# Kernel optimization log

Measured on AMD Instinct MI355X. Metric: run time of the kernel, lower is better.

## Reference

```python
import jax, jax.numpy as jnp
import numpy as np

T, B, E, H = 2048, 2, 1024, 16
HD = E // H

def setup_inputs() -> dict:
    key = jax.random.key(0)
    k1, k2, k3 = jax.random.split(key, 3)
    x = jax.random.normal(k1, (T, B, E), dtype=jnp.float32)
    # xavier-uniform-like scale for weights
    in_proj_w = jax.random.normal(k2, (3 * E, E), dtype=jnp.float32) * (2.0 / (4 * E)) ** 0.5
    in_proj_b = jnp.zeros((3 * E,), dtype=jnp.float32)
    out_w = jax.random.normal(k3, (E, E), dtype=jnp.float32) * (1.0 / E) ** 0.5
    out_b = jnp.zeros((E,), dtype=jnp.float32)
    return {"x": x, "in_proj_w": in_proj_w, "in_proj_b": in_proj_b, "out_w": out_w, "out_b": out_b}

def reference(x, in_proj_w, in_proj_b, out_w, out_b):
    t, b, e = x.shape
    scale = HD ** (-0.5)
    # fused QKV projection: F.linear(x, W, b) = x @ W.T + b
    qkv = x @ in_proj_w.T + in_proj_b            # [T, B, 3E]
    q, k, v = jnp.split(qkv, 3, axis=-1)         # each [T, B, E]
    q = q * scale
    # reshape to heads: [T, B, E] -> [B, H, T, HD]
    def to_heads(a):
        return a.reshape(t, b, H, HD).transpose(1, 2, 0, 3)
    qh, kh, vh = to_heads(q), to_heads(k), to_heads(v)
    # scores [B, H, T, T] -- full NxN materialization, same as torch.bmm
    scores = jnp.einsum('bhtd,bhsd->bhts', qh, kh)
    w = jax.nn.softmax(scores.astype(jnp.float32), axis=-1).astype(scores.dtype)
    attn = jnp.einsum('bhts,bhsd->bhtd', w, vh)  # [B, H, T, HD]
    attn = attn.transpose(2, 0, 1, 3).reshape(t, b, e)  # [T, B, E]
    attn = attn @ out_w.T + out_b
    attn_weights = w.sum(axis=1) / H             # [B, T, T] head-averaged
    return attn, attn_weights
```

## Files before the change

### kernel.cpp

```cpp
#include <hip/hip_runtime.h>
#include <hip/hip_bf16.h>
#include <cstdint>

#define T_DIM 2048
#define B_DIM 2
#define E_DIM 1024
#define H_DIM 16
#define HD_DIM 64
#define M_DIM 4096
#define N1_DIM 3072
#define QK_SCALE 0.125f

typedef __attribute__((ext_vector_type(8))) short bfrag;
typedef __attribute__((ext_vector_type(4))) float f32x4;

__device__ __forceinline__ short f2bf(float f) {
  union { float f; uint32_t u; } v; v.f = f;
  uint32_t r = v.u + 0x7fffu + ((v.u >> 16) & 1u);
  return (short)(r >> 16);
}
__device__ __forceinline__ float bf2f(short b) {
  union { uint32_t u; float f; } v; v.u = ((uint32_t)(uint16_t)b) << 16;
  return v.f;
}
__device__ __forceinline__ f32x4 mfma16(bfrag a, bfrag b, f32x4 c) {
  return __builtin_amdgcn_mfma_f32_16x16x32_bf16(a, b, c, 0, 0, 0);
}

__global__ void split_kernel(const float* __restrict__ in,
                             short* __restrict__ hi, short* __restrict__ lo, int n) {
  int i = blockIdx.x * blockDim.x + threadIdx.x;
  int stride = gridDim.x * blockDim.x;
  for (; i < n; i += stride) {
    float v = in[i];
    short h = f2bf(v);
    hi[i] = h;
    lo[i] = f2bf(v - bf2f(h));
  }
}

template<int N_T, int K_T, bool OUT_BF16, bool DO_SCALE>
__global__ __launch_bounds__(256) void gemm_split(
    const short* __restrict__ Ahi, const short* __restrict__ Alo,
    const short* __restrict__ Bhi, const short* __restrict__ Blo,
    const float* __restrict__ bias, void* __restrict__ Cout)
{
  constexpr int BK = 32;
  constexpr int LDT = BK + 8;
  __shared__ short As[2][128][LDT];
  __shared__ short Bs[2][128][LDT];

  const int m0 = blockIdx.y * 128;
  const int n0 = blockIdx.x * 128;
  const int tid = threadIdx.x;
  const int lane = tid & 63;
  const int wave = tid >> 6;
  const int wr = (wave >> 1) * 64;
  const int wc = (wave & 1) * 64;

  f32x4 acc[4][4];
#pragma unroll
  for (int i = 0; i < 4; ++i)
#pragma unroll
    for (int j = 0; j < 4; ++j) acc[i][j] = f32x4{0.f, 0.f, 0.f, 0.f};

  const int ldr = tid >> 1;
  const int ldc0 = (tid & 1) << 4;

  for (int k0 = 0; k0 < K_T; k0 += BK) {
    const size_t aoff = (size_t)(m0 + ldr) * K_T + k0 + ldc0;
    const size_t boff = (size_t)(n0 + ldr) * K_T + k0 + ldc0;
    bfrag ah0 = *(const bfrag*)(Ahi + aoff);
    bfrag ah1 = *(const bfrag*)(Ahi + aoff + 8);
    bfrag al0 = *(const bfrag*)(Alo + aoff);
    bfrag al1 = *(const bfrag*)(Alo + aoff + 8);
    bfrag bh0 = *(const bfrag*)(Bhi + boff);
    bfrag bh1 = *(const bfrag*)(Bhi + boff + 8);
    bfrag bl0 = *(const bfrag*)(Blo + boff);
    bfrag bl1 = *(const bfrag*)(Blo + boff + 8);
    __syncthreads();
    *(bfrag*)&As[0][ldr][ldc0]     = ah0;
    *(bfrag*)&As[0][ldr][ldc0 + 8] = ah1;
    *(bfrag*)&As[1][ldr][ldc0]     = al0;
    *(bfrag*)&As[1][ldr][ldc0 + 8] = al1;
    *(bfrag*)&Bs[0][ldr][ldc0]     = bh0;
    *(bfrag*)&Bs[0][ldr][ldc0 + 8] = bh1;
    *(bfrag*)&Bs[1][ldr][ldc0]     = bl0;
    *(bfrag*)&Bs[1][ldr][ldc0 + 8] = bl1;
    __syncthreads();

    const int fr = lane & 15;
    const int fk = (lane >> 4) << 3;
    bfrag afh[4], afl[4];
#pragma unroll
    for (int fi = 0; fi < 4; ++fi) {
      afh[fi] = *(const bfrag*)&As[0][wr + fi * 16 + fr][fk];
      afl[fi] = *(const bfrag*)&As[1][wr + fi * 16 + fr][fk];
    }
#pragma unroll
    for (int fj = 0; fj < 4; ++fj) {
      bfrag bfh = *(const bfrag*)&Bs[0][wc + fj * 16 + fr][fk];
      bfrag bfl = *(const bfrag*)&Bs[1][wc + fj * 16 + fr][fk];
#pragma unroll
      for (int fi = 0; fi < 4; ++fi) {
        acc[fi][fj] = mfma16(afh[fi], bfh, acc[fi][fj]);
        acc[fi][fj] = mfma16(afh[fi], bfl, acc[fi][fj]);
        acc[fi][fj] = mfma16(afl[fi], bfh, acc[fi][fj]);
      }
    }
  }

  const int cr = (lane >> 4) << 2;
  const int cc = lane & 15;
#pragma unroll
  for (int fi = 0; fi < 4; ++fi)
#pragma unroll
    for (int fj = 0; fj < 4; ++fj)
#pragma unroll
      for (int r = 0; r < 4; ++r) {
        int m = m0 + wr + fi * 16 + cr + r;
        int n = n0 + wc + fj * 16 + cc;
        float v = acc[fi][fj][r] + bias[n];
        if (DO_SCALE) { if (n < E_DIM) v *= QK_SCALE; }
        if (OUT_BF16) ((short*)Cout)[(size_t)m * N_T + n] = f2bf(v);
        else          ((float*)Cout)[(size_t)m * N_T + n] = v;
      }
}

__global__ __launch_bounds__(256) void attn_kernel(
    const short* __restrict__ qkv,
    float* __restrict__ linv_ws,
    short* __restrict__ ctx_hi, short* __restrict__ ctx_lo)
{
  __shared__ short Ks[64][72];
  __shared__ short Vt[64][72];
  __shared__ short Ps[64][72];
  __shared__ float l_lds[64];

  const int bh = blockIdx.x;
  const int b  = bh >> 4;
  const int h  = bh & 15;
  const int t0 = blockIdx.y * 64;
  const int tid  = threadIdx.x;
  const int lane = tid & 63;
  const int wave = tid >> 6;
  const int fr = lane & 15;
  const int fk = (lane >> 4) << 3;
  const int cr = (lane >> 4) << 2;

  const size_t qb = ((size_t)(t0 + wave * 16 + fr) * B_DIM + b) * N1_DIM + h * HD_DIM;
  const bfrag aq0 = *(const bfrag*)(qkv + qb + fk);
  const bfrag aq1 = *(const bfrag*)(qkv + qb + fk + 32);

  if (tid < 64) l_lds[tid] = 0.0f;

  f32x4 pv[4];
#pragma unroll
  for (int i = 0; i < 4; ++i) pv[i] = f32x4{0.f, 0.f, 0.f, 0.f};

  const int r  = tid >> 2;
  const int ds = (tid & 3) << 4;
  const int vc0 = (((r >> 3) ^ (ds >> 3)) << 3) | (r & 7);
  const int vc1 = (((r >> 3) ^ ((ds >> 3) + 1)) << 3) | (r & 7);

  const size_t kstep = ((size_t)64 * B_DIM) * N1_DIM;
  size_t kb = ((size_t)r * B_DIM + b) * N1_DIM + E_DIM + h * HD_DIM + ds;
  bfrag kv0 = *(const bfrag*)(qkv + kb);
  bfrag kv1 = *(const bfrag*)(qkv + kb + 8);
  bfrag vv0 = *(const bfrag*)(qkv + kb + E_DIM);
  bfrag vv1 = *(const bfrag*)(qkv + kb + E_DIM + 8);

  for (int st = 0; st < T_DIM / 64; ++st) {
    __syncthreads();
    *(bfrag*)&Ks[r][ds]     = kv0;
    *(bfrag*)&Ks[r][ds + 8] = kv1;
#pragma unroll
    for (int j = 0; j < 8; ++j) Vt[ds + j][vc0]     = vv0[j];
#pragma unroll
    for (int j = 0; j < 8; ++j) Vt[ds + 8 + j][vc1] = vv1[j];
    __syncthreads();

    f32x4 sacc[4];
    __builtin_amdgcn_s_setprio(1);
#pragma unroll
    for (int fs = 0; fs < 4; ++fs) {
      bfrag bk0 = *(const bfrag*)&Ks[fs * 16 + fr][fk];
      bfrag bk1 = *(const bfrag*)&Ks[fs * 16 + fr][fk + 32];
      f32x4 a = f32x4{0.f, 0.f, 0.f, 0.f};
      a = mfma16(aq0, bk0, a);
      a = mfma16(aq1, bk1, a);
      sacc[fs] = a;
    }
    __builtin_amdgcn_s_setprio(0);

    if (st + 1 < T_DIM / 64) {
      kb += kstep;
      kv0 = *(const bfrag*)(qkv + kb);
      kv1 = *(const bfrag*)(qkv + kb + 8);
      vv0 = *(const bfrag*)(qkv + kb + E_DIM);
      vv1 = *(const bfrag*)(qkv + kb + E_DIM + 8);
    }

    float rsum[4] = {0.f, 0.f, 0.f, 0.f};
#pragma unroll
    for (int fs = 0; fs < 4; ++fs) {
#pragma unroll
      for (int rr = 0; rr < 4; ++rr) {
        float p = __expf(sacc[fs][rr]);
        Ps[wave * 16 + cr + rr][fs * 16 + fr] = f2bf(p);
        rsum[rr] += p;
      }
    }
#pragma unroll
    for (int rr = 0; rr < 4; ++rr) {
      float v = rsum[rr];
      v += __shfl_xor(v, 1);
      v += __shfl_xor(v, 2);
      v += __shfl_xor(v, 4);
      v += __shfl_xor(v, 8);
      if (fr == 0) l_lds[wave * 16 + cr + rr] += v;
    }

    bfrag pa0 = *(const bfrag*)&Ps[wave * 16 + fr][fk];
    bfrag pa1 = *(const bfrag*)&Ps[wave * 16 + fr][fk + 32];
    __builtin_amdgcn_s_setprio(1);
#pragma unroll
    for (int fd = 0; fd < 4; ++fd) {
      const int R = fd * 16 + fr;
      const int sg = (R >> 3) & 7;
      bfrag bv0 = *(const bfrag*)&Vt[R][(((fk >> 3) ^ sg) << 3)];
      bfrag bv1 = *(const bfrag*)&Vt[R][((((fk >> 3) + 4) ^ sg) << 3)];
      pv[fd] = mfma16(pa0, bv0, pv[fd]);
      pv[fd] = mfma16(pa1, bv1, pv[fd]);
    }
    __builtin_amdgcn_s_setprio(0);
  }
  __syncthreads();

  if (tid < 64) linv_ws[(size_t)bh * T_DIM + t0 + tid] = 1.0f / l_lds[tid];
#pragma unroll
  for (int rr = 0; rr < 4; ++rr) {
    const int row = wave * 16 + cr + rr;
    const float inv = 1.0f / l_lds[row];
#pragma unroll
    for (int fd = 0; fd < 4; ++fd) {
      float v = pv[fd][rr] * inv;
      int d = fd * 16 + fr;
      size_t off = ((size_t)(t0 + row) * B_DIM + b) * E_DIM + h * HD_DIM + d;
      short hi = f2bf(v);
      ctx_hi[off] = hi;
      ctx_lo[off] = f2bf(v - bf2f(hi));
    }
  }
}

__global__ __launch_bounds__(256) void weights_kernel(
    const short* __restrict__ qkv, const float* __restrict__ linv,
    float* __restrict__ outw)
{
  __shared__ short Qs[64][72];
  __shared__ short Ks[64][72];
  __shared__ float Ls[16][64];

  const int s0 = blockIdx.x * 64;
  const int bt = blockIdx.y;
  const int b  = bt >> 5;
  const int t0 = (bt & 31) * 64;
  const int tid  = threadIdx.x;
  const int lane = tid & 63;
  const int wave = tid >> 6;
  const int fr = lane & 15;
  const int fk = (lane >> 4) << 3;
  const int cr = (lane >> 4) << 2;

  {
    const int h  = tid >> 4;
    const int r4 = (tid & 15) << 2;
    float4 v = *(const float4*)(linv + (size_t)(b * H_DIM + h) * T_DIM + t0 + r4);
    Ls[h][r4 + 0] = v.x * (1.0f / H_DIM);
    Ls[h][r4 + 1] = v.y * (1.0f / H_DIM);
    Ls[h][r4 + 2] = v.z * (1.0f / H_DIM);
    Ls[h][r4 + 3] = v.w * (1.0f / H_DIM);
  }

  f32x4 wacc[4];
#pragma unroll
  for (int i = 0; i < 4; ++i) wacc[i] = f32x4{0.f, 0.f, 0.f, 0.f};

  const int r  = tid >> 2;
  const int ds = (tid & 3) << 4;

  for (int h = 0; h < H_DIM; ++h) {
    const size_t qbase = ((size_t)(t0 + r) * B_DIM + b) * N1_DIM + h * HD_DIM + ds;
    const size_t kbase = ((size_t)(s0 + r) * B_DIM + b) * N1_DIM + E_DIM + h * HD_DIM + ds;
    bfrag q0 = *(const bfrag*)(qkv + qbase);
    bfrag q1 = *(const bfrag*)(qkv + qbase + 8);
    bfrag k0 = *(const bfrag*)(qkv + kbase);
    bfrag k1 = *(const bfrag*)(qkv + kbase + 8);
    __syncthreads();
    *(bfrag*)&Qs[r][ds]     = q0;
    *(bfrag*)&Qs[r][ds + 8] = q1;
    *(bfrag*)&Ks[r][ds]     = k0;
    *(bfrag*)&Ks[r][ds + 8] = k1;
    __syncthreads();

    bfrag aq0 = *(const bfrag*)&Qs[wave * 16 + fr][fk];
    bfrag aq1 = *(const bfrag*)&Qs[wave * 16 + fr][fk + 32];
#pragma unroll
    for (int fs = 0; fs < 4; ++fs) {
      bfrag bk0 = *(const bfrag*)&Ks[fs * 16 + fr][fk];
      bfrag bk1 = *(const bfrag*)&Ks[fs * 16 + fr][fk + 32];
      f32x4 a = f32x4{0.f, 0.f, 0.f, 0.f};
      a = mfma16(aq0, bk0, a);
      a = mfma16(aq1, bk1, a);
#pragma unroll
      for (int rr = 0; rr < 4; ++rr)
        wacc[fs][rr] += __expf(a[rr]) * Ls[h][wave * 16 + cr + rr];
    }
  }

#pragma unroll
  for (int fs = 0; fs < 4; ++fs)
#pragma unroll
    for (int rr = 0; rr < 4; ++rr) {
      const int t = t0 + wave * 16 + cr + rr;
      outw[((size_t)b * T_DIM + t) * T_DIM + s0 + fs * 16 + fr] = wacc[fs][rr];
    }
}

extern "C" void kernel_launch(void* const* d_in, const int* in_sizes, int n_in,
                              void* d_out, int out_size, void* d_ws, size_t ws_size,
                              hipStream_t stream) {
  const float* x  = (const float*)d_in[0];
  const float* w1 = (const float*)d_in[1];
  const float* b1 = (const float*)d_in[2];
  const float* w2 = (const float*)d_in[3];
  const float* b2 = (const float*)d_in[4];
  float* out = (float*)d_out;

  char* ws = (char*)d_ws;
  size_t off = 0;
  auto carve = [&](size_t bytes) -> void* {
    void* p = ws + off;
    off = (off + bytes + 255) & ~(size_t)255;
    return p;
  };
  short* x_hi  = (short*)carve((size_t)M_DIM * E_DIM * 2);
  short* x_lo  = (short*)carve((size_t)M_DIM * E_DIM * 2);
  short* w1_hi = (short*)carve((size_t)N1_DIM * E_DIM * 2);
  short* w1_lo = (short*)carve((size_t)N1_DIM * E_DIM * 2);
  short* w2_hi = (short*)carve((size_t)E_DIM * E_DIM * 2);
  short* w2_lo = (short*)carve((size_t)E_DIM * E_DIM * 2);
  short* qkv   = (short*)carve((size_t)M_DIM * N1_DIM * 2);
  float* linv  = (float*)carve((size_t)B_DIM * H_DIM * T_DIM * 4);
  short* c_hi  = (short*)carve((size_t)M_DIM * E_DIM * 2);
  short* c_lo  = (short*)carve((size_t)M_DIM * E_DIM * 2);

  split_kernel<<<2048, 256, 0, stream>>>(x,  x_hi,  x_lo,  M_DIM * E_DIM);
  split_kernel<<<2048, 256, 0, stream>>>(w1, w1_hi, w1_lo, N1_DIM * E_DIM);
  split_kernel<<<1024, 256, 0, stream>>>(w2, w2_hi, w2_lo, E_DIM * E_DIM);

  gemm_split<N1_DIM, E_DIM, true, true><<<dim3(N1_DIM / 128, M_DIM / 128), 256, 0, stream>>>(
      x_hi, x_lo, w1_hi, w1_lo, b1, (void*)qkv);

  attn_kernel<<<dim3(B_DIM * H_DIM, T_DIM / 64), 256, 0, stream>>>(
      qkv, linv, c_hi, c_lo);

  weights_kernel<<<dim3(T_DIM / 64, B_DIM * (T_DIM / 64)), 256, 0, stream>>>(
      qkv, linv, out + (size_t)M_DIM * E_DIM);

  gemm_split<E_DIM, E_DIM, false, false><<<dim3(E_DIM / 128, M_DIM / 128), 256, 0, stream>>>(
      c_hi, c_lo, w2_hi, w2_lo, b2, (void*)out);
}
```

Before: 372.4 us.

## Double-buffer K/V tiles, widen attention blocks to 128 queries, MFMA row sums

The attention kernel now gives each block 128 query rows, two 16-row fragments per wave, so every K/V tile loaded into LDS serves twice as many queries. K/V tiles are double-buffered in LDS, which cuts the per-tile barriers from two to one and lets the next tile's store overlap with compute. Row sums of the softmax numerators are now computed with an MFMA against a vector of bf16 ones, replacing the shuffle reduction and the shared l_lds accumulator. In exchange the grid is half as large, register and LDS use per block go up, and the sums are now taken over bf16-rounded probabilities.

```diff
diff --git a/kernel.cpp b/kernel.cpp
--- a/kernel.cpp
+++ b/kernel.cpp
@@ -132,15 +132,14 @@
     float* __restrict__ linv_ws,
     short* __restrict__ ctx_hi, short* __restrict__ ctx_lo)
 {
-  __shared__ short Ks[64][72];
-  __shared__ short Vt[64][72];
-  __shared__ short Ps[64][72];
-  __shared__ float l_lds[64];
+  __shared__ short Ks[2][64][72];
+  __shared__ short Vt[2][64][72];
+  __shared__ short Ps[128][76];
 
   const int bh = blockIdx.x;
   const int b  = bh >> 4;
   const int h  = bh & 15;
-  const int t0 = blockIdx.y * 64;
+  const int t0 = blockIdx.y * 128;
   const int tid  = threadIdx.x;
   const int lane = tid & 63;
   const int wave = tid >> 6;
@@ -148,52 +147,81 @@
   const int fk = (lane >> 4) << 3;
   const int cr = (lane >> 4) << 2;
 
-  const size_t qb = ((size_t)(t0 + wave * 16 + fr) * B_DIM + b) * N1_DIM + h * HD_DIM;
-  const bfrag aq0 = *(const bfrag*)(qkv + qb + fk);
-  const bfrag aq1 = *(const bfrag*)(qkv + qb + fk + 32);
-
-  if (tid < 64) l_lds[tid] = 0.0f;
-
-  f32x4 pv[4];
-#pragma unroll
-  for (int i = 0; i < 4; ++i) pv[i] = f32x4{0.f, 0.f, 0.f, 0.f};
+  bfrag aq[2][2];
+#pragma unroll
+  for (int hh = 0; hh < 2; ++hh) {
+    const size_t qb = ((size_t)(t0 + 32 * wave + 16 * hh + fr) * B_DIM + b) * N1_DIM + h * HD_DIM;
+    aq[hh][0] = *(const bfrag*)(qkv + qb + fk);
+    aq[hh][1] = *(const bfrag*)(qkv + qb + fk + 32);
+  }
+
+  bfrag ones;
+#pragma unroll
+  for (int j = 0; j < 8; ++j) ones[j] = (short)0x3F80;
+
+  f32x4 pv[2][4];
+  f32x4 pvsum[2];
+#pragma unroll
+  for (int hh = 0; hh < 2; ++hh) {
+    pvsum[hh] = f32x4{0.f, 0.f, 0.f, 0.f};
+#pragma unroll
+    for (int fd = 0; fd < 4; ++fd) pv[hh][fd] = f32x4{0.f, 0.f, 0.f, 0.f};
+  }
 
   const int r  = tid >> 2;
   const int ds = (tid & 3) << 4;
   const int vc0 = (((r >> 3) ^ (ds >> 3)) << 3) | (r & 7);
   const int vc1 = (((r >> 3) ^ ((ds >> 3) + 1)) << 3) | (r & 7);
 
+  constexpr int NT = T_DIM / 64;
   const size_t kstep = ((size_t)64 * B_DIM) * N1_DIM;
   size_t kb = ((size_t)r * B_DIM + b) * N1_DIM + E_DIM + h * HD_DIM + ds;
+
   bfrag kv0 = *(const bfrag*)(qkv + kb);
   bfrag kv1 = *(const bfrag*)(qkv + kb + 8);
   bfrag vv0 = *(const bfrag*)(qkv + kb + E_DIM);
   bfrag vv1 = *(const bfrag*)(qkv + kb + E_DIM + 8);
-
-  for (int st = 0; st < T_DIM / 64; ++st) {
-    __syncthreads();
-    *(bfrag*)&Ks[r][ds]     = kv0;
-    *(bfrag*)&Ks[r][ds + 8] = kv1;
-#pragma unroll
-    for (int j = 0; j < 8; ++j) Vt[ds + j][vc0]     = vv0[j];
-#pragma unroll
-    for (int j = 0; j < 8; ++j) Vt[ds + 8 + j][vc1] = vv1[j];
-    __syncthreads();
-
-    f32x4 sacc[4];
+  *(bfrag*)&Ks[0][r][ds]     = kv0;
+  *(bfrag*)&Ks[0][r][ds + 8] = kv1;
+#pragma unroll
+  for (int j = 0; j < 8; ++j) Vt[0][ds + j][vc0]     = vv0[j];
+#pragma unroll
+  for (int j = 0; j < 8; ++j) Vt[0][ds + 8 + j][vc1] = vv1[j];
+  kb += kstep;
+  kv0 = *(const bfrag*)(qkv + kb);
+  kv1 = *(const bfrag*)(qkv + kb + 8);
+  vv0 = *(const bfrag*)(qkv + kb + E_DIM);
+  vv1 = *(const bfrag*)(qkv + kb + E_DIM + 8);
+
+  for (int st = 0; st < NT; ++st) {
+    const int p = st & 1;
+    __syncthreads();
+
+    f32x4 sacc[2][4];
     __builtin_amdgcn_s_setprio(1);
 #pragma unroll
     for (int fs = 0; fs < 4; ++fs) {
-      bfrag bk0 = *(const bfrag*)&Ks[fs * 16 + fr][fk];
-      bfrag bk1 = *(const bfrag*)&Ks[fs * 16 + fr][fk + 32];
-      f32x4 a = f32x4{0.f, 0.f, 0.f, 0.f};
-      a = mfma16(aq0, bk0, a);
-      a = mfma16(aq1, bk1, a);
-      sacc[fs] = a;
+      bfrag bk0 = *(const bfrag*)&Ks[p][fs * 16 + fr][fk];
+      bfrag bk1 = *(const bfrag*)&Ks[p][fs * 16 + fr][fk + 32];
+#pragma unroll
+      for (int hh = 0; hh < 2; ++hh) {
+        f32x4 a = f32x4{0.f, 0.f, 0.f, 0.f};
+        a = mfma16(aq[hh][0], bk0, a);
+        a = mfma16(aq[hh][1], bk1, a);
+        sacc[hh][fs] = a;
+      }
     }
     __builtin_amdgcn_s_setprio(0);
 
-    if (st + 1 < T_DIM / 64) {
+    if (st + 1 < NT) {
+      *(bfrag*)&Ks[p ^ 1][r][ds]     = kv0;
+      *(bfrag*)&Ks[p ^ 1][r][ds + 8] = kv1;
+#pragma unroll
+      for (int j = 0; j < 8; ++j) Vt[p ^ 1][ds + j][vc0]     = vv0[j];
+#pragma unroll
+      for (int j = 0; j < 8; ++j) Vt[p ^ 1][ds + 8 + j][vc1] = vv1[j];
+    }
+    if (st + 2 < NT) {
       kb += kstep;
       kv0 = *(const bfrag*)(qkv + kb);
       kv1 = *(const bfrag*)(qkv + kb + 8);
@@ -201,57 +229,49 @@
       vv1 = *(const bfrag*)(qkv + kb + E_DIM + 8);
     }
 
-    float rsum[4] = {0.f, 0.f, 0.f, 0.f};
-#pragma unroll
-    for (int fs = 0; fs < 4; ++fs) {
-#pragma unroll
-      for (int rr = 0; rr < 4; ++rr) {
-        float p = __expf(sacc[fs][rr]);
-        Ps[wave * 16 + cr + rr][fs * 16 + fr] = f2bf(p);
-        rsum[rr] += p;
-      }
-    }
+#pragma unroll
+    for (int hh = 0; hh < 2; ++hh) {
+#pragma unroll
+      for (int fs = 0; fs < 4; ++fs)
+#pragma unroll
+        for (int rr = 0; rr < 4; ++rr)
+          Ps[32 * wave + 16 * hh + cr + rr][fs * 16 + fr] = f2bf(__expf(sacc[hh][fs][rr]));
+
+      bfrag pa0 = *(const bfrag*)&Ps[32 * wave + 16 * hh + fr][fk];
+      bfrag pa1 = *(const bfrag*)&Ps[32 * wave + 16 * hh + fr][fk + 32];
+      pvsum[hh] = mfma16(pa0, ones, pvsum[hh]);
+      pvsum[hh] = mfma16(pa1, ones, pvsum[hh]);
+      __builtin_amdgcn_s_setprio(1);
+#pragma unroll
+      for (int fd = 0; fd < 4; ++fd) {
+        const int R = fd * 16 + fr;
+        const int sg = (R >> 3) & 7;
+        bfrag bv0 = *(const bfrag*)&Vt[p][R][(((fk >> 3) ^ sg) << 3)];
+        bfrag bv1 = *(const bfrag*)&Vt[p][R][((((fk >> 3) + 4) ^ sg) << 3)];
+        pv[hh][fd] = mfma16(pa0, bv0, pv[hh][fd]);
+        pv[hh][fd] = mfma16(pa1, bv1, pv[hh][fd]);
+      }
+      __builtin_amdgcn_s_setprio(0);
+    }
+  }
+
+#pragma unroll
+  for (int hh = 0; hh < 2; ++hh)
 #pragma unroll
     for (int rr = 0; rr < 4; ++rr) {
-      float v = rsum[rr];
-      v += __shfl_xor(v, 1);
-      v += __shfl_xor(v, 2);
-      v += __shfl_xor(v, 4);
-      v += __shfl_xor(v, 8);
-      if (fr == 0) l_lds[wave * 16 + cr + rr] += v;
-    }
-
-    bfrag pa0 = *(const bfrag*)&Ps[wave * 16 + fr][fk];
-    bfrag pa1 = *(const bfrag*)&Ps[wave * 16 + fr][fk + 32];
-    __builtin_amdgcn_s_setprio(1);
-#pragma unroll
-    for (int fd = 0; fd < 4; ++fd) {
-      const int R = fd * 16 + fr;
-      const int sg = (R >> 3) & 7;
-      bfrag bv0 = *(const bfrag*)&Vt[R][(((fk >> 3) ^ sg) << 3)];
-      bfrag bv1 = *(const bfrag*)&Vt[R][((((fk >> 3) + 4) ^ sg) << 3)];
-      pv[fd] = mfma16(pa0, bv0, pv[fd]);
-      pv[fd] = mfma16(pa1, bv1, pv[fd]);
-    }
-    __builtin_amdgcn_s_setprio(0);
-  }
-  __syncthreads();
-
-  if (tid < 64) linv_ws[(size_t)bh * T_DIM + t0 + tid] = 1.0f / l_lds[tid];
-#pragma unroll
-  for (int rr = 0; rr < 4; ++rr) {
-    const int row = wave * 16 + cr + rr;
-    const float inv = 1.0f / l_lds[row];
-#pragma unroll
-    for (int fd = 0; fd < 4; ++fd) {
-      float v = pv[fd][rr] * inv;
-      int d = fd * 16 + fr;
-      size_t off = ((size_t)(t0 + row) * B_DIM + b) * E_DIM + h * HD_DIM + d;
-      short hi = f2bf(v);
-      ctx_hi[off] = hi;
-      ctx_lo[off] = f2bf(v - bf2f(hi));
-    }
-  }
+      const int row = 32 * wave + 16 * hh + cr + rr;
+      const float inv = 1.0f / pvsum[hh][rr];
+      if (fr == 0) linv_ws[(size_t)bh * T_DIM + t0 + row] = inv;
+#pragma unroll
+      for (int fd = 0; fd < 4; ++fd) {
+        float v = pv[hh][fd][rr] * inv;
+        int d = fd * 16 + fr;
+        size_t off = ((size_t)(t0 + row) * B_DIM + b) * E_DIM + h * HD_DIM + d;
+        short hi = f2bf(v);
+        ctx_hi[off] = hi;
+        ctx_lo[off] = f2bf(v - bf2f(hi));
+      }
+    }
 }
 
 __global__ __launch_bounds__(256) void weights_kernel(
@@ -363,7 +383,7 @@
   gemm_split<N1_DIM, E_DIM, true, true><<<dim3(N1_DIM / 128, M_DIM / 128), 256, 0, stream>>>(
       x_hi, x_lo, w1_hi, w1_lo, b1, (void*)qkv);
 
-  attn_kernel<<<dim3(B_DIM * H_DIM, T_DIM / 64), 256, 0, stream>>>(
+  attn_kernel<<<dim3(B_DIM * H_DIM, T_DIM / 128), 256, 0, stream>>>(
       qkv, linv, c_hi, c_lo);
 
   weights_kernel<<<dim3(T_DIM / 64, B_DIM * (T_DIM / 64)), 256, 0, stream>>>(
```

Measured after the change: 339.8 us. 1.1x faster.
